# Optimization experiments

Hardware: AMD Instinct MI355X
Metric: run time of the kernel (lower is better)

Reference implementation:

```python
import jax, jax.numpy as jnp
import numpy as np

B, L = 2, 2048          # batch, seq len (self-attention: M == L)
H, D, NB = 8, 16, 8     # n_heads, clifford_dim, n_blades (2^3 for sig_g=[1,1,1])
DM = H * D * NB         # d_model = 1024

# reverse() signs per blade for a 3D algebra, blade grades [0,1,1,1,2,2,2,3]:
# (-1)^{k(k-1)/2}; Euclidean metric signs from get_blade_signs are all +1,
# so the combined twist q_w = reverse(q) * signs is just these per-blade signs.
REV_SIGNS = jnp.array([1., 1., 1., 1., -1., -1., -1., -1.], dtype=jnp.float32)


def setup_inputs() -> dict:
    key = jax.random.key(0)
    ks = jax.random.split(key, 7)
    s = 1.0 / np.sqrt(DM)
    return {
        "query": jax.random.normal(ks[0], (B, L, DM), dtype=jnp.float32),
        "Wq": jax.random.normal(ks[1], (DM, DM), dtype=jnp.float32) * s,
        "bq": jax.random.normal(ks[2], (DM,), dtype=jnp.float32) * s,
        "Wk": jax.random.normal(ks[3], (DM, DM), dtype=jnp.float32) * s,
        "bk": jax.random.normal(ks[4], (DM,), dtype=jnp.float32) * s,
        "Wv": jax.random.normal(ks[5], (DM, DM), dtype=jnp.float32) * s,
        "bv": jax.random.normal(ks[6], (DM,), dtype=jnp.float32) * s,
    }


def reference(query, Wq, bq, Wk, bk, Wv, bv):
    b, l, _ = query.shape
    # projections (torch Linear: x @ W^T + b), reshape to (B,H,L,D,NB)
    def proj(x, W, bias):
        y = x @ W.T + bias
        return y.reshape(b, l, H, D, NB).transpose(0, 2, 1, 3, 4)

    q = proj(query, Wq, bq)
    k = proj(query, Wk, bk)   # self-attention: key = value = query
    v = proj(query, Wv, bv)

    q_w = q * REV_SIGNS  # reverse + blade-sign twist (elementwise over blade axis)
    scale = 1.0 / np.sqrt(D * NB)
    logits = jnp.einsum('bhldi,bhmdi->bhlm', q_w, k) * scale
    attn = jax.nn.softmax(logits, axis=-1)
    out = jnp.einsum('bhlm,bhmdi->bhldi', attn, v)
    out = out.transpose(0, 2, 1, 3, 4).reshape(b, l, -1)
    return out, attn.mean(axis=1)  # need_weights=True path
```

## Files before the change

kernel.cpp:

```cpp
#include <hip/hip_runtime.h>

typedef __attribute__((ext_vector_type(8))) __bf16 bf16x8;
typedef __attribute__((ext_vector_type(4))) __bf16 bf16x4;
typedef __attribute__((ext_vector_type(4))) float f32x4;
typedef __attribute__((ext_vector_type(16))) float f32x16;
typedef __attribute__((ext_vector_type(8))) unsigned short us8;
typedef __attribute__((ext_vector_type(4))) unsigned int u32x4;

constexpr float SCALE_L2E = 0.08838834764831845f * 1.4426950408889634f;

__device__ __forceinline__ unsigned short f2bf(float f) {
  unsigned int u = __float_as_uint(f);
  u = (u + 0x7FFFu + ((u >> 16) & 1u)) >> 16;
  return (unsigned short)u;
}

__device__ __forceinline__ void gl_lds16(const void* g, void* l) {
  __builtin_amdgcn_global_load_lds(
      (__attribute__((address_space(1))) void*)const_cast<void*>(g),
      (__attribute__((address_space(3))) void*)l, 16, 0, 0);
}

__global__ __launch_bounds__(256) void k_convert(
    const float* __restrict__ q, const float* __restrict__ wq,
    const float* __restrict__ wk, const float* __restrict__ wv,
    unsigned short* __restrict__ xb, unsigned short* __restrict__ wb) {
  long i = ((long)blockIdx.x * 256 + threadIdx.x) * 8;
  const float* s; unsigned short* d;
  if (i < 4194304)      { s = q  + i;             d = xb + i; }
  else if (i < 5242880) { s = wq + (i - 4194304); d = wb + (i - 4194304); }
  else if (i < 6291456) { s = wk + (i - 5242880); d = wb + 1048576 + (i - 5242880); }
  else                  { s = wv + (i - 6291456); d = wb + 2097152 + (i - 6291456); }
  float4 a = *(const float4*)s;
  float4 b = *(const float4*)(s + 4);
  us8 r;
  r[0]=f2bf(a.x); r[1]=f2bf(a.y); r[2]=f2bf(a.z); r[3]=f2bf(a.w);
  r[4]=f2bf(b.x); r[5]=f2bf(b.y); r[6]=f2bf(b.z); r[7]=f2bf(b.w);
  *(us8*)d = r;
}

__global__ __launch_bounds__(256) void k_proj(
    const unsigned short* __restrict__ xb, const unsigned short* __restrict__ wb,
    const float* __restrict__ bq, const float* __restrict__ bk, const float* __restrict__ bv,
    unsigned short* __restrict__ oq, unsigned short* __restrict__ ok_, unsigned short* __restrict__ vt) {
  __shared__ unsigned short As[4096];
  __shared__ unsigned short Bs[4096];
  const int t = threadIdx.x;
  const int wave = t >> 6, lane = t & 63;
  const int lrow = lane & 15, grp = lane >> 4;
  const int z = blockIdx.z;
  const unsigned short* w = wb + (size_t)z * 1048576;
  const float* bias = (z == 0) ? bq : ((z == 1) ? bk : bv);

  const unsigned short* asrc = xb + ((size_t)(blockIdx.y * 128 + (t >> 2)) * 1024 + (t & 3) * 8);
  const unsigned short* bsrc = w  + ((size_t)(blockIdx.x * 128 + (t >> 2)) * 1024 + (t & 3) * 8);

  f32x4 acc[4][4] = {};
  for (int kt = 0; kt < 32; ++kt) {
    gl_lds16(asrc + kt*32,              &As[t*8]);
    gl_lds16(asrc + kt*32 + 64*1024,    &As[2048 + t*8]);
    gl_lds16(bsrc + kt*32,              &Bs[t*8]);
    gl_lds16(bsrc + kt*32 + 64*1024,    &Bs[2048 + t*8]);
    __syncthreads();
    const int wr = wave >> 1, wc = wave & 1;
    bf16x8 af[4], bf[4];
#pragma unroll
    for (int mf = 0; mf < 4; ++mf)
      af[mf] = *(const bf16x8*)&As[(wr*64 + mf*16 + lrow)*32 + grp*8];
#pragma unroll
    for (int nf = 0; nf < 4; ++nf)
      bf[nf] = *(const bf16x8*)&Bs[(wc*64 + nf*16 + lrow)*32 + grp*8];
#pragma unroll
    for (int mf = 0; mf < 4; ++mf)
#pragma unroll
      for (int nf = 0; nf < 4; ++nf)
        acc[mf][nf] = __builtin_amdgcn_mfma_f32_16x16x32_bf16(af[mf], bf[nf], acc[mf][nf], 0, 0, 0);
    __syncthreads();
  }
  const int wr = wave >> 1, wc = wave & 1;
  if (z == 2) {
#pragma unroll
    for (int nf = 0; nf < 4; ++nf) {
      const int col = blockIdx.x*128 + wc*64 + nf*16 + lrow;
      const int h = col >> 7, dd = col & 127;
      const int dt = dd >> 5, lv = dd & 31;
      const float bsv = bias[col];
#pragma unroll
      for (int mf = 0; mf < 4; ++mf) {
        const int r0 = blockIdx.y*128 + wr*64 + mf*16 + grp*4;
        const int bb = r0 >> 11, m = r0 & 2047;
        const int mc = m >> 4, him = (m >> 3) & 1, j0 = m & 7;
        bf16x4 pv;
#pragma unroll
        for (int i = 0; i < 4; ++i) pv[i] = (__bf16)(acc[mf][nf][i] + bsv);
        const size_t off = ((((size_t)((bb*8 + h)*4 + dt))*128 + mc)*64 + lv + 32*him)*8 + j0;
        *(bf16x4*)&vt[off] = pv;
      }
    }
  } else {
    unsigned short* dst = (z == 0) ? oq : ok_;
    const float sign = (z == 0 && (lane & 7) >= 4) ? -1.0f : 1.0f;
#pragma unroll
    for (int nf = 0; nf < 4; ++nf) {
      const int col = blockIdx.x*128 + wc*64 + nf*16 + lrow;
      const float bsv = bias[col];
#pragma unroll
      for (int mf = 0; mf < 4; ++mf)
#pragma unroll
        for (int i = 0; i < 4; ++i) {
          const int row = blockIdx.y*128 + wr*64 + mf*16 + grp*4 + i;
          dst[(size_t)row*1024 + col] = f2bf((acc[mf][nf][i] + bsv) * sign);
        }
    }
  }
}

__global__ __launch_bounds__(256) void k_repack(const unsigned short* __restrict__ kws,
                                                unsigned short* __restrict__ kfrag) {
  const int c = blockIdx.x * 256 + threadIdx.x;
  const int lane = c & 63, kc = (c >> 6) & 7, mtile = (c >> 9) & 63, bh = c >> 15;
  const int b = bh >> 3, h = bh & 7;
  const int m = mtile*32 + (lane & 31);
  const int kd = kc*16 + (lane >> 5)*8;
  us8 v = *(const us8*)&kws[((size_t)(b*2048 + m))*1024 + h*128 + kd];
  *(us8*)&kfrag[(size_t)c * 8] = v;
}

__global__ __launch_bounds__(256) void k_attn_out(
    const unsigned short* __restrict__ qw, const unsigned short* __restrict__ kfrag,
    const unsigned short* __restrict__ vfrag, float* __restrict__ outp,
    float* __restrict__ rsw) {
  __shared__ __align__(16) char pool[65536];
  unsigned short (*KsL)[8192] = (unsigned short(*)[8192])pool;
  unsigned short (*VsL)[8192] = (unsigned short(*)[8192])(pool + 32768);
  float (*slab)[32][36] = (float(*)[32][36])pool;
  float (*rsred)[32] = (float(*)[32])(pool + 61440);
  float* invb = (float*)(pool + 62464);

  const int bid = blockIdx.x;
  const int xcd = bid & 7, r_ = bid >> 3;
  const int bh = (xcd << 1) | (r_ & 1);
  const int lt = r_ >> 1;
  const int b = bh >> 3, h = bh & 7;
  const int t = threadIdx.x;
  const int wave = t >> 6, lane = t & 63;
  const int mg = wave >> 1, lg = wave & 1;
  const int lm = lane & 31, hi = lane >> 5;

  bf16x8 qf[8];
  {
    const unsigned short* qp = qw + ((size_t)(b*2048 + lt*64 + lg*32 + lm))*1024
                                  + (size_t)h*128 + hi*8;
#pragma unroll
    for (int kc = 0; kc < 8; ++kc) qf[kc] = *(const bf16x8*)(qp + kc*16);
  }

  const unsigned short* kbp = kfrag + (size_t)bh*262144;
  const unsigned short* vbp = vfrag + (size_t)bh*262144;
  const int vdt = (t >> 6) & 3, vln = (t & 63) * 8;

  auto STAGE = [&](int buf, int it) {
#pragma unroll
    for (int q = 0; q < 2; ++q)
#pragma unroll
      for (int p = 0; p < 2; ++p)
        gl_lds16(kbp + (q*32 + it)*4096 + (p*256 + t)*8, &KsL[buf][q*4096 + (p*256 + t)*8]);
#pragma unroll
    for (int s = 0; s < 2; ++s)
#pragma unroll
      for (int w2 = 0; w2 < 2; ++w2)
        gl_lds16(vbp + vdt*65536 + (s*64 + it*2 + w2)*512 + vln,
                 &VsL[buf][s*4096 + w2*2048 + vdt*512 + vln]);
  };

  f32x16 oacc[4] = {};
  float rs = 0.f;

  STAGE(0, 0);
  __syncthreads();

  for (int it = 0; it < 32; ++it) {
    const int cur = it & 1;
    if (it + 1 < 32) STAGE(cur ^ 1, it + 1);

    bf16x8 kf[8];
#pragma unroll
    for (int kc = 0; kc < 8; ++kc)
      kf[kc] = *(const bf16x8*)&KsL[cur][mg*4096 + kc*512 + lane*8];
    f32x16 s = {};
#pragma unroll
    for (int kc = 0; kc < 8; ++kc)
      s = __builtin_amdgcn_mfma_f32_32x32x16_bf16(kf[kc], qf[kc], s, 0, 0, 0);

    bf16x8 vf[8];
#pragma unroll
    for (int w2 = 0; w2 < 2; ++w2)
#pragma unroll
      for (int dt = 0; dt < 4; ++dt)
        vf[w2*4 + dt] = *(const bf16x8*)&VsL[cur][mg*4096 + w2*2048 + dt*512 + lane*8];

    float e[16];
#pragma unroll
    for (int r = 0; r < 16; ++r) e[r] = __builtin_amdgcn_exp2f(s[r] * SCALE_L2E);
    float ps = 0.f;
#pragma unroll
    for (int r = 0; r < 16; ++r) ps += e[r];
    rs += ps;

    bf16x8 pf[2];
#pragma unroll
    for (int w2 = 0; w2 < 2; ++w2) {
      unsigned a0, a1, b0, b1;
      asm("v_cvt_pk_bf16_f32 %0, %1, %2" : "=v"(a0) : "v"(e[8*w2+0]), "v"(e[8*w2+1]));
      asm("v_cvt_pk_bf16_f32 %0, %1, %2" : "=v"(a1) : "v"(e[8*w2+2]), "v"(e[8*w2+3]));
      asm("v_cvt_pk_bf16_f32 %0, %1, %2" : "=v"(b0) : "v"(e[8*w2+4]), "v"(e[8*w2+5]));
      asm("v_cvt_pk_bf16_f32 %0, %1, %2" : "=v"(b1) : "v"(e[8*w2+6]), "v"(e[8*w2+7]));
      asm("v_permlane32_swap_b32 %0, %1" : "+v"(a0), "+v"(b0));
      asm("v_permlane32_swap_b32 %0, %1" : "+v"(a1), "+v"(b1));
      u32x4 pw = {a0, a1, b0, b1};
      pf[w2] = __builtin_bit_cast(bf16x8, pw);
    }

#pragma unroll
    for (int dt = 0; dt < 4; ++dt) {
      oacc[dt] = __builtin_amdgcn_mfma_f32_32x32x16_bf16(vf[dt],     pf[0], oacc[dt], 0, 0, 0);
      oacc[dt] = __builtin_amdgcn_mfma_f32_32x32x16_bf16(vf[4 + dt], pf[1], oacc[dt], 0, 0, 0);
    }
    __syncthreads();
  }

  rs += __shfl_xor(rs, 32, 64);
  if (lane < 32) rsred[wave][lm] = rs;
  __syncthreads();
  if (t < 64) {
    const int tlg = t >> 5, tl = t & 31;
    const float tot = rsred[tlg][tl] + rsred[2 + tlg][tl];
    rsw[(size_t)bh*2048 + lt*64 + t] = tot;
    invb[t] = 1.0f / tot;
  }

#pragma unroll
  for (int dt = 0; dt < 4; ++dt) {
    __syncthreads();
#pragma unroll
    for (int c = 0; c < 4; ++c) {
      float4 v4 = { oacc[dt][4*c + 0], oacc[dt][4*c + 1], oacc[dt][4*c + 2], oacc[dt][4*c + 3] };
      *(float4*)&slab[wave][lm][8*c + 4*hi] = v4;
    }
    __syncthreads();
    const int lgg = t >> 7, idx = t & 127;
    const int l = idx >> 2, d0 = (idx & 3) * 8;
    const float iv = invb[lgg*32 + l];
    float4 x0 = *(const float4*)&slab[lgg][l][d0];
    float4 x1 = *(const float4*)&slab[lgg][l][d0 + 4];
    float4 y0 = *(const float4*)&slab[2 + lgg][l][d0];
    float4 y1 = *(const float4*)&slab[2 + lgg][l][d0 + 4];
    float4 o0 = { (x0.x + y0.x)*iv, (x0.y + y0.y)*iv, (x0.z + y0.z)*iv, (x0.w + y0.w)*iv };
    float4 o1 = { (x1.x + y1.x)*iv, (x1.y + y1.y)*iv, (x1.z + y1.z)*iv, (x1.w + y1.w)*iv };
    float* op = outp + ((size_t)(b*2048 + lt*64 + lgg*32 + l))*1024 + h*128 + dt*32 + d0;
    *(float4*)op = o0;
    *(float4*)(op + 4) = o1;
  }
}

__global__ __launch_bounds__(256) void k_attn_mean(
    const unsigned short* __restrict__ qw, const unsigned short* __restrict__ kb,
    const float* __restrict__ rsw, float* __restrict__ meanp) {
  __shared__ unsigned short Qs[128*128];
  __shared__ unsigned short Ks[128*128];
  __shared__ float inv_s[8*128];
  const int mt = blockIdx.x;
  const int lt = blockIdx.y;
  const int b  = blockIdx.z;
  const int t = threadIdx.x;
  const int wave = t >> 6, lane = t & 63;
  const int lrow = lane & 15, grp = lane >> 4;
  const int wl = wave >> 1, wm = wave & 1;
  const int trow = t >> 4;
  const int tcol = t & 15;

  for (int idx = t; idx < 1024; idx += 256) {
    int hh = idx >> 7, ll = idx & 127;
    inv_s[idx] = 1.0f / rsw[(size_t)(b*8 + hh)*2048 + lt*128 + ll];
  }

  f32x4 acc[4][4] = {};

  for (int h = 0; h < 8; ++h) {
    __syncthreads();
    const unsigned short* qbase = qw + ((size_t)(b*2048 + lt*128) * 1024 + h*128);
    const unsigned short* kbase = kb + ((size_t)(b*2048 + mt*128) * 1024 + h*128);
#pragma unroll
    for (int i = 0; i < 8; ++i) {
      const int row = i*16 + trow;
      const int sc = (tcol ^ (row & 7)) * 8;
      gl_lds16(qbase + (size_t)row*1024 + sc, &Qs[i*2048 + t*8]);
      gl_lds16(kbase + (size_t)row*1024 + sc, &Ks[i*2048 + t*8]);
    }
    __syncthreads();

    f32x4 s[4][4] = {};
#pragma unroll
    for (int ks = 0; ks < 4; ++ks) {
      bf16x8 af[4], bf[4];
#pragma unroll
      for (int lf = 0; lf < 4; ++lf) {
        const int row = wl*64 + lf*16 + lrow;
        af[lf] = *(const bf16x8*)&Qs[row*128 + ((ks*32 + grp*8) ^ ((row & 7) << 3))];
      }
#pragma unroll
      for (int mf = 0; mf < 4; ++mf) {
        const int row = wm*64 + mf*16 + lrow;
        bf[mf] = *(const bf16x8*)&Ks[row*128 + ((ks*32 + grp*8) ^ ((row & 7) << 3))];
      }
#pragma unroll
      for (int lf = 0; lf < 4; ++lf)
#pragma unroll
        for (int mf = 0; mf < 4; ++mf)
          s[lf][mf] = __builtin_amdgcn_mfma_f32_16x16x32_bf16(af[lf], bf[mf], s[lf][mf], 0, 0, 0);
    }
#pragma unroll
    for (int lf = 0; lf < 4; ++lf)
#pragma unroll
      for (int i = 0; i < 4; ++i) {
        const float iv = inv_s[h*128 + wl*64 + lf*16 + grp*4 + i];
#pragma unroll
        for (int mf = 0; mf < 4; ++mf)
          acc[lf][mf][i] += __builtin_amdgcn_exp2f(s[lf][mf][i] * SCALE_L2E) * iv;
      }
  }

#pragma unroll
  for (int lf = 0; lf < 4; ++lf)
#pragma unroll
    for (int i = 0; i < 4; ++i) {
      const int l = lt*128 + wl*64 + lf*16 + grp*4 + i;
      const size_t rowo = (size_t)(b*2048 + l) * 2048;
#pragma unroll
      for (int mf = 0; mf < 4; ++mf)
        meanp[rowo + mt*128 + wm*64 + mf*16 + lrow] = acc[lf][mf][i] * 0.125f;
    }
}

extern "C" void kernel_launch(void* const* d_in, const int* in_sizes, int n_in,
                              void* d_out, int out_size, void* d_ws, size_t ws_size,
                              hipStream_t stream) {
  (void)in_sizes; (void)n_in; (void)out_size; (void)ws_size;
  const float* query = (const float*)d_in[0];
  const float* Wq = (const float*)d_in[1];
  const float* bq = (const float*)d_in[2];
  const float* Wk = (const float*)d_in[3];
  const float* bk = (const float*)d_in[4];
  const float* Wv = (const float*)d_in[5];
  const float* bv = (const float*)d_in[6];
  float* outp  = (float*)d_out;
  float* meanp = outp + 4194304;

  char* ws = (char*)d_ws;
  unsigned short* xb    = (unsigned short*)(ws);
  unsigned short* wb    = (unsigned short*)(ws + 8388608);
  unsigned short* qws   = (unsigned short*)(ws + 14680064);
  unsigned short* kws   = (unsigned short*)(ws + 23068672);
  unsigned short* kfrag = (unsigned short*)(ws + 31457280);
  unsigned short* vfrag = (unsigned short*)(ws + 39845888);
  float*          rsw   = (float*)(ws + 48234496);

  k_convert<<<3584, 256, 0, stream>>>(query, Wq, Wk, Wv, xb, wb);
  k_proj<<<dim3(8, 32, 3), 256, 0, stream>>>(xb, wb, bq, bk, bv, qws, kws, vfrag);
  k_repack<<<2048, 256, 0, stream>>>(kws, kfrag);
  k_attn_out<<<512, 256, 0, stream>>>(qws, kfrag, vfrag, outp, rsw);
  k_attn_mean<<<dim3(16, 16, 2), 256, 0, stream>>>(qws, kws, rsw, meanp);
}
```

Before: 136.7 us.

## Restructure attention-mean kernel: one wave per head, 32x32 MFMA on repacked K fragments

Rewrites the head-averaged attention kernel so each 512-thread block handles 32 query rows for all 8 heads, one wave per head. Q fragments stay in registers, and pre-repacked K fragments are streamed into LDS per 32-column tile using 32x32x16 MFMAs. The cross-head sum is done through an LDS slab, with the next K tile staged while the current tile is reduced. The block-to-batch/column-slice mapping is tied to XCD index. This is meant to cut redundant Q loads and the swizzled LDS staging of the old 128x128 tiling, at the cost of more barriers and smaller tiles per block.

```diff
diff --git a/kernel.cpp b/kernel.cpp
--- a/kernel.cpp
+++ b/kernel.cpp
@@ -263,83 +263,84 @@
   }
 }
 
-__global__ __launch_bounds__(256) void k_attn_mean(
-    const unsigned short* __restrict__ qw, const unsigned short* __restrict__ kb,
+__global__ __launch_bounds__(512) void k_attn_mean(
+    const unsigned short* __restrict__ qw, const unsigned short* __restrict__ kfrag,
     const float* __restrict__ rsw, float* __restrict__ meanp) {
-  __shared__ unsigned short Qs[128*128];
-  __shared__ unsigned short Ks[128*128];
-  __shared__ float inv_s[8*128];
-  const int mt = blockIdx.x;
-  const int lt = blockIdx.y;
-  const int b  = blockIdx.z;
+  __shared__ unsigned short KsL[32768];
+  __shared__ float slab[8][32][36];
+  __shared__ float inv_s[256];
+  const int bid = blockIdx.x;
+  const int xcd = bid & 7, lt = bid >> 3;
+  const int b = xcd >> 2, ms = xcd & 3;
   const int t = threadIdx.x;
-  const int wave = t >> 6, lane = t & 63;
-  const int lrow = lane & 15, grp = lane >> 4;
-  const int wl = wave >> 1, wm = wave & 1;
-  const int trow = t >> 4;
-  const int tcol = t & 15;
-
-  for (int idx = t; idx < 1024; idx += 256) {
-    int hh = idx >> 7, ll = idx & 127;
-    inv_s[idx] = 1.0f / rsw[(size_t)(b*8 + hh)*2048 + lt*128 + ll];
-  }
-
-  f32x4 acc[4][4] = {};
-
-  for (int h = 0; h < 8; ++h) {
-    __syncthreads();
-    const unsigned short* qbase = qw + ((size_t)(b*2048 + lt*128) * 1024 + h*128);
-    const unsigned short* kbase = kb + ((size_t)(b*2048 + mt*128) * 1024 + h*128);
+  const int h = t >> 6, lane = t & 63;
+  const int lm = lane & 31, hi = lane >> 5;
+
+  if (t < 256) inv_s[t] = 1.0f / rsw[(size_t)(b*8 + (t>>5))*2048 + lt*32 + (t&31)];
+
+  bf16x8 qf[8];
+  {
+    const unsigned short* qp = qw + ((size_t)(b*2048 + lt*32 + lm))*1024 + h*128 + hi*8;
+#pragma unroll
+    for (int kc = 0; kc < 8; ++kc) qf[kc] = *(const bf16x8*)(qp + kc*16);
+  }
+
+  auto STAGE = [&](int it) {
 #pragma unroll
     for (int i = 0; i < 8; ++i) {
-      const int row = i*16 + trow;
-      const int sc = (tcol ^ (row & 7)) * 8;
-      gl_lds16(qbase + (size_t)row*1024 + sc, &Qs[i*2048 + t*8]);
-      gl_lds16(kbase + (size_t)row*1024 + sc, &Ks[i*2048 + t*8]);
-    }
-    __syncthreads();
-
-    f32x4 s[4][4] = {};
-#pragma unroll
-    for (int ks = 0; ks < 4; ++ks) {
-      bf16x8 af[4], bf[4];
-#pragma unroll
-      for (int lf = 0; lf < 4; ++lf) {
-        const int row = wl*64 + lf*16 + lrow;
-        af[lf] = *(const bf16x8*)&Qs[row*128 + ((ks*32 + grp*8) ^ ((row & 7) << 3))];
-      }
-#pragma unroll
-      for (int mf = 0; mf < 4; ++mf) {
-        const int row = wm*64 + mf*16 + lrow;
-        bf[mf] = *(const bf16x8*)&Ks[row*128 + ((ks*32 + grp*8) ^ ((row & 7) << 3))];
-      }
-#pragma unroll
-      for (int lf = 0; lf < 4; ++lf)
-#pragma unroll
-        for (int mf = 0; mf < 4; ++mf)
-          s[lf][mf] = __builtin_amdgcn_mfma_f32_16x16x32_bf16(af[lf], bf[mf], s[lf][mf], 0, 0, 0);
-    }
-#pragma unroll
-    for (int lf = 0; lf < 4; ++lf)
-#pragma unroll
-      for (int i = 0; i < 4; ++i) {
-        const float iv = inv_s[h*128 + wl*64 + lf*16 + grp*4 + i];
-#pragma unroll
-        for (int mf = 0; mf < 4; ++mf)
-          acc[lf][mf][i] += __builtin_amdgcn_exp2f(s[lf][mf][i] * SCALE_L2E) * iv;
-      }
-  }
-
-#pragma unroll
-  for (int lf = 0; lf < 4; ++lf)
-#pragma unroll
-    for (int i = 0; i < 4; ++i) {
-      const int l = lt*128 + wl*64 + lf*16 + grp*4 + i;
-      const size_t rowo = (size_t)(b*2048 + l) * 2048;
-#pragma unroll
-      for (int mf = 0; mf < 4; ++mf)
-        meanp[rowo + mt*128 + wm*64 + mf*16 + lrow] = acc[lf][mf][i] * 0.125f;
-    }
+      const int c = i*512 + t;
+      const int hh = c >> 9;
+      gl_lds16(kfrag + (size_t)(b*8 + hh)*262144 + (size_t)(ms*16 + it)*4096 + (c & 511)*8,
+               &KsL[c*8]);
+    }
+  };
+
+  auto REDUCE = [&](int it) {
+    const int m = t & 31, lp = t >> 5;
+#pragma unroll
+    for (int j = 0; j < 2; ++j) {
+      const int l = lp*2 + j;
+      float sum = 0.f;
+#pragma unroll
+      for (int w = 0; w < 8; ++w) sum += slab[w][m][l];
+      meanp[(size_t)(b*2048 + lt*32 + l)*2048 + (ms*16 + it)*32 + m] = sum * 0.125f;
+    }
+  };
+
+  STAGE(0);
+  __syncthreads();
+
+  float iv_r[16];
+#pragma unroll
+  for (int r = 0; r < 16; ++r)
+    iv_r[r] = inv_s[h*32 + ((r & 3) + 8*(r >> 2) + 4*hi)];
+
+  for (int it = 0; it < 16; ++it) {
+    bf16x8 kf[8];
+#pragma unroll
+    for (int kc = 0; kc < 8; ++kc)
+      kf[kc] = *(const bf16x8*)&KsL[(h*8 + kc)*512 + lane*8];
+    f32x16 s = {};
+#pragma unroll
+    for (int kc = 0; kc < 8; ++kc)
+      s = __builtin_amdgcn_mfma_f32_32x32x16_bf16(qf[kc], kf[kc], s, 0, 0, 0);
+
+    float e[16];
+#pragma unroll
+    for (int r = 0; r < 16; ++r)
+      e[r] = __builtin_amdgcn_exp2f(s[r] * SCALE_L2E) * iv_r[r];
+
+#pragma unroll
+    for (int gq = 0; gq < 4; ++gq) {
+      float4 v4 = { e[gq*4 + 0], e[gq*4 + 1], e[gq*4 + 2], e[gq*4 + 3] };
+      *(float4*)&slab[h][lm][gq*8 + hi*4] = v4;
+    }
+    __syncthreads();
+
+    if (it + 1 < 16) STAGE(it + 1);
+    REDUCE(it);
+    __syncthreads();
+  }
 }
 
 extern "C" void kernel_launch(void* const* d_in, const int* in_sizes, int n_in,
@@ -369,5 +370,5 @@
   k_proj<<<dim3(8, 32, 3), 256, 0, stream>>>(xb, wb, bq, bk, bv, qws, kws, vfrag);
   k_repack<<<2048, 256, 0, stream>>>(kws, kfrag);
   k_attn_out<<<512, 256, 0, stream>>>(qws, kfrag, vfrag, outp, rsw);
-  k_attn_mean<<<dim3(16, 16, 2), 256, 0, stream>>>(qws, kws, rsw, meanp);
-}
+  k_attn_mean<<<512, 512, 0, stream>>>(qws, kfrag, rsw, meanp);
+}
```

Result: slower. 149.3 us (+9.3%).
